# Optimization experiments

Hardware: AMD Instinct MI355X
Metric: run time of the kernel (lower is better)

The kernel has to match this reference:

```python
import jax, jax.numpy as jnp
import numpy as np

B, T, H, D, O = 2, 2048, 16, 64, 1024  # batch, seq, heads, head_size, output_size
E = H * D


def setup_inputs() -> dict:
    key = jax.random.key(0)
    ks = jax.random.split(key, 8)
    return {
        "query": jax.random.normal(ks[0], (B, T, E), jnp.float32),
        "key": jax.random.normal(ks[1], (B, T, E), jnp.float32),
        "value": jax.random.normal(ks[2], (B, T, E), jnp.float32),
        "Wq": jax.random.normal(ks[3], (E, E), jnp.float32) * (E ** -0.5),
        "Wk": jax.random.normal(ks[4], (E, E), jnp.float32) * (E ** -0.5),
        "Wv": jax.random.normal(ks[5], (E, E), jnp.float32) * (E ** -0.5),
        "proj_kernel": jax.random.normal(ks[6], (H, D, O), jnp.float32) * (D ** -0.5),
        "proj_bias": jax.random.normal(ks[7], (O,), jnp.float32),
    }


def reference(query, key, value, Wq, Wk, Wv, proj_kernel, proj_bias):
    # Linear projections (torch nn.Linear: x @ W.T), then split heads
    q = (query @ Wq.T).reshape(B, T, H, D)
    k = (key @ Wk.T).reshape(B, T, H, D)
    v = (value @ Wv.T).reshape(B, T, H, D)
    q = q * (D ** -0.5)  # scale query by 1/sqrt(head_size)
    # logits: [B, H, N, M]
    logits = jnp.einsum("bnhd,bmhd->bhnm", q, k)
    attn_coef = jax.nn.softmax(logits, axis=-1)
    # attn @ V -> [B, N, H, D]
    mh = jnp.einsum("bhnm,bmhd->bnhd", attn_coef, v)
    # custom output projection with per-head kernel [H, D, O]
    out = jnp.einsum("bnhd,hdo->bno", mh, proj_kernel) + proj_bias
    return out, attn_coef
```

## Files before the change

kernel.cpp:

```cpp
#include <hip/hip_runtime.h>
#include <hip/hip_bf16.h>
#include <math.h>

#define B_ 2
#define T_ 2048
#define H_ 16
#define D_ 64
#define E_ 1024
#define O_ 1024
#define BT_ 4096
#define SCALE_Q 0.18033688011f

typedef __attribute__((ext_vector_type(8))) short bf8;
typedef __attribute__((ext_vector_type(4))) float f4;

static __device__ __forceinline__ unsigned short f2bf(float f) {
  unsigned u = __builtin_bit_cast(unsigned, f);
  u += 0x7FFFu + ((u >> 16) & 1u);
  return (unsigned short)(u >> 16);
}

static __device__ __forceinline__ uint4 cvt8(float4 a, float4 b) {
  union { unsigned short s[8]; uint4 v; } u;
  u.s[0] = f2bf(a.x); u.s[1] = f2bf(a.y); u.s[2] = f2bf(a.z); u.s[3] = f2bf(a.w);
  u.s[4] = f2bf(b.x); u.s[5] = f2bf(b.y); u.s[6] = f2bf(b.z); u.s[7] = f2bf(b.w);
  return u.v;
}

static __device__ __forceinline__ f4 mfma16(bf8 a, bf8 b, f4 c) {
  return __builtin_amdgcn_mfma_f32_16x16x32_bf16(a, b, c, 0, 0, 0);
}

static __device__ __forceinline__ float ex2(float x) {
  float r;
  asm("v_exp_f32 %0, %1" : "=v"(r) : "v"(x));
  return r;
}

static __device__ __forceinline__ unsigned cvtpk_bf(float lo, float hi) {
  unsigned r;
  asm("v_cvt_pk_bf16_f32 %0, %1, %2" : "=v"(r) : "v"(lo), "v"(hi));
  return r;
}

__global__ __launch_bounds__(256) void qkv_gemm(const float* __restrict__ Xq,
                                                const float* __restrict__ Xk,
                                                const float* __restrict__ Xv,
                                                const float* __restrict__ Wq,
                                                const float* __restrict__ Wk,
                                                const float* __restrict__ Wv,
                                                unsigned short* __restrict__ dq,
                                                unsigned short* __restrict__ dk,
                                                unsigned short* __restrict__ dv) {
  __shared__ __align__(16) unsigned short lA[64 * 40];
  __shared__ __align__(16) unsigned short lB[128 * 40];
  const int z = blockIdx.z;
  const float* X = (z == 0) ? Xq : (z == 1) ? Xk : Xv;
  const float* W = (z == 0) ? Wq : (z == 1) ? Wk : Wv;
  unsigned short* dst = (z == 0) ? dq : (z == 1) ? dk : dv;
  const float scale = (z == 0) ? SCALE_Q : 1.0f;

  const int tid = threadIdx.x;
  const int bx = blockIdx.x, by = blockIdx.y;
  const int lane = tid & 63, w = tid >> 6;
  const int l15 = lane & 15, qd = lane >> 4;
  const int wr = (w >> 1) * 32, wc = (w & 1) * 64;

  const int ar = tid >> 2, akc = (tid & 3) << 3;
  const int br = tid >> 1, bkc = (tid & 1) << 4;
  const float* aptr = X + (size_t)(bx * 64 + ar) * E_ + akc;
  const float* bptr = W + (size_t)(by * 128 + br) * E_ + bkc;

  f4 acc[2][4];
#pragma unroll
  for (int i = 0; i < 2; ++i)
#pragma unroll
    for (int j = 0; j < 4; ++j) acc[i][j] = (f4){0.f, 0.f, 0.f, 0.f};

  for (int k0 = 0; k0 < E_; k0 += 32) {
    __syncthreads();
    {
      const float4* p = (const float4*)aptr;
      *(uint4*)&lA[ar * 40 + akc] = cvt8(p[0], p[1]);
    }
    {
      const float4* p = (const float4*)bptr;
      *(uint4*)&lB[br * 40 + bkc] = cvt8(p[0], p[1]);
      *(uint4*)&lB[br * 40 + bkc + 8] = cvt8(p[2], p[3]);
    }
    aptr += 32; bptr += 32;
    __syncthreads();

    bf8 af[2], bfr[4];
#pragma unroll
    for (int rt = 0; rt < 2; ++rt)
      af[rt] = *(const bf8*)&lA[(wr + rt * 16 + l15) * 40 + qd * 8];
#pragma unroll
    for (int ct = 0; ct < 4; ++ct)
      bfr[ct] = *(const bf8*)&lB[(wc + ct * 16 + l15) * 40 + qd * 8];
#pragma unroll
    for (int rt = 0; rt < 2; ++rt)
#pragma unroll
      for (int ct = 0; ct < 4; ++ct)
        acc[rt][ct] = mfma16(af[rt], bfr[ct], acc[rt][ct]);
  }

#pragma unroll
  for (int rt = 0; rt < 2; ++rt)
#pragma unroll
    for (int ct = 0; ct < 4; ++ct)
#pragma unroll
      for (int r = 0; r < 4; ++r) {
        int m = bx * 64 + wr + rt * 16 + qd * 4 + r;
        int n = by * 128 + wc + ct * 16 + l15;
        int b = m >> 11, t = m & 2047;
        int h = n >> 6, d = n & 63;
        dst[((size_t)(b * H_ + h) * T_ + t) * D_ + d] = f2bf(acc[rt][ct][r] * scale);
      }
}

__global__ __launch_bounds__(256) void transpose_v(const unsigned short* __restrict__ vh,
                                                   unsigned short* __restrict__ vt) {
  __shared__ __align__(16) unsigned short lT[64 * 72];
  const int tid = threadIdx.x;
  const int bh = blockIdx.x >> 5;
  const int t0 = (blockIdx.x & 31) * 64;
  const unsigned short* src = vh + (size_t)bh * T_ * D_ + (size_t)t0 * D_;
#pragma unroll
  for (int i = 0; i < 2; ++i) {
    int c = tid + i * 256;
    int row = c >> 3, dc = (c & 7) << 3;
    *(uint4*)&lT[row * 72 + dc] = *(const uint4*)(src + row * D_ + dc);
  }
  __syncthreads();
  unsigned short* dstp = vt + (size_t)bh * D_ * T_;
#pragma unroll
  for (int i = 0; i < 2; ++i) {
    int c = tid + i * 256;
    int d = c >> 3, tc = (c & 7) << 3;
    union { unsigned short s[8]; uint4 v; } u;
#pragma unroll
    for (int j = 0; j < 8; ++j) u.s[j] = lT[(tc + j) * 72 + d];
    *(uint4*)(dstp + (size_t)d * T_ + t0 + tc) = u.v;
  }
}

__global__ __launch_bounds__(256) void transpose_proj(const float* __restrict__ pk,
                                                      unsigned short* __restrict__ pt) {
  __shared__ __align__(16) unsigned short lT[64 * 72];
  const int tid = threadIdx.x;
  const int hd0 = (blockIdx.x >> 4) * 64;
  const int o0 = (blockIdx.x & 15) * 64;
#pragma unroll
  for (int i = 0; i < 2; ++i) {
    int c = tid + i * 256;
    int row = c >> 3, oc = (c & 7) << 3;
    const float4* p = (const float4*)(pk + (size_t)(hd0 + row) * O_ + o0 + oc);
    *(uint4*)&lT[row * 72 + oc] = cvt8(p[0], p[1]);
  }
  __syncthreads();
#pragma unroll
  for (int i = 0; i < 2; ++i) {
    int c = tid + i * 256;
    int orow = c >> 3, hc = (c & 7) << 3;
    union { unsigned short s[8]; uint4 v; } u;
#pragma unroll
    for (int j = 0; j < 8; ++j) u.s[j] = lT[(hc + j) * 72 + orow];
    *(uint4*)(pt + (size_t)(o0 + orow) * E_ + hd0 + hc) = u.v;
  }
}

__global__ __launch_bounds__(256) void attention(const unsigned short* __restrict__ qh,
                                                 const unsigned short* __restrict__ kh,
                                                 const unsigned short* __restrict__ vt,
                                                 float* __restrict__ attn,
                                                 unsigned short* __restrict__ mh) {
  __shared__ __align__(16) unsigned short lK[64 * 72];
  __shared__ __align__(16) unsigned short lV[64 * 72];
  __shared__ __align__(16) unsigned short lP[4 * 16 * 72];

  const int tid = threadIdx.x;
  const int bh = blockIdx.x >> 5;
  const int n0 = (blockIdx.x & 31) * 64;
  const int lane = tid & 63, w = tid >> 6;
  const int l15 = lane & 15, qd = lane >> 4;

  const unsigned short* qbase = qh + ((size_t)bh * T_ + n0) * D_;
  const unsigned short* kbase = kh + (size_t)bh * T_ * D_;
  const unsigned short* vbase = vt + (size_t)bh * D_ * T_;

  const bf8 aq0 = *(const bf8*)(qbase + (w * 16 + l15) * D_ + qd * 8);
  const bf8 aq1 = *(const bf8*)(qbase + (w * 16 + l15) * D_ + 32 + qd * 8);

  const int srow = tid >> 3, scol = (tid & 7) << 3;

  float mL = -INFINITY, lL = 0.f;
  for (int m0 = 0; m0 < T_; m0 += 64) {
    __syncthreads();
#pragma unroll
    for (int i = 0; i < 2; ++i) {
      int row = srow + i * 32;
      *(uint4*)&lK[row * 72 + scol] = *(const uint4*)(kbase + (size_t)(m0 + row) * D_ + scol);
    }
    __syncthreads();
    f4 s[4];
#pragma unroll
    for (int kk = 0; kk < 4; ++kk) {
      bf8 k0 = *(const bf8*)&lK[(kk * 16 + l15) * 72 + qd * 8];
      bf8 k1 = *(const bf8*)&lK[(kk * 16 + l15) * 72 + 32 + qd * 8];
      f4 t = (f4){0.f, 0.f, 0.f, 0.f};
      t = mfma16(k0, aq0, t);
      t = mfma16(k1, aq1, t);
      s[kk] = t;
    }
    float tm = s[0][0];
#pragma unroll
    for (int kk = 0; kk < 4; ++kk)
#pragma unroll
      for (int r = 0; r < 4; ++r) tm = fmaxf(tm, s[kk][r]);
    float nm = fmaxf(mL, tm);
    lL *= ex2(mL - nm);
    mL = nm;
#pragma unroll
    for (int kk = 0; kk < 4; ++kk)
#pragma unroll
      for (int r = 0; r < 4; ++r) lL += ex2(s[kk][r] - mL);
  }

  float mrow = mL, lrow = lL;
#pragma unroll
  for (int off = 16; off < 64; off <<= 1) {
    float om = __shfl_xor(mrow, off);
    float ol = __shfl_xor(lrow, off);
    float nm = fmaxf(mrow, om);
    lrow = lrow * ex2(mrow - nm) + ol * ex2(om - nm);
    mrow = nm;
  }
  const float invl = 1.0f / lrow;

  f4 o[4];
#pragma unroll
  for (int dt = 0; dt < 4; ++dt) o[dt] = (f4){0.f, 0.f, 0.f, 0.f};

  float* attnrow = attn + ((size_t)bh * T_ + n0 + w * 16 + l15) * T_ + qd * 4;
  unsigned short* lPw = lP + w * 16 * 72;

  for (int m0 = 0; m0 < T_; m0 += 64) {
    __syncthreads();
#pragma unroll
    for (int i = 0; i < 2; ++i) {
      int row = srow + i * 32;
      *(uint4*)&lK[row * 72 + scol] = *(const uint4*)(kbase + (size_t)(m0 + row) * D_ + scol);
      *(uint4*)&lV[row * 72 + scol] = *(const uint4*)(vbase + (size_t)row * T_ + m0 + scol);
    }
    __syncthreads();
    f4 s[4];
#pragma unroll
    for (int kk = 0; kk < 4; ++kk) {
      bf8 k0 = *(const bf8*)&lK[(kk * 16 + l15) * 72 + qd * 8];
      bf8 k1 = *(const bf8*)&lK[(kk * 16 + l15) * 72 + 32 + qd * 8];
      f4 t = (f4){0.f, 0.f, 0.f, 0.f};
      t = mfma16(k0, aq0, t);
      t = mfma16(k1, aq1, t);
      s[kk] = t;
    }
#pragma unroll
    for (int kk = 0; kk < 4; ++kk) {
      float p0 = ex2(s[kk][0] - mrow) * invl;
      float p1 = ex2(s[kk][1] - mrow) * invl;
      float p2 = ex2(s[kk][2] - mrow) * invl;
      float p3 = ex2(s[kk][3] - mrow) * invl;
      f4 pf = (f4){p0, p1, p2, p3};
      __builtin_nontemporal_store(pf, (f4*)(attnrow + m0 + kk * 16));
      uint2 pb;
      pb.x = cvtpk_bf(p0, p1);
      pb.y = cvtpk_bf(p2, p3);
      *(uint2*)&lPw[l15 * 72 + kk * 16 + qd * 4] = pb;
    }
    bf8 ap0 = *(const bf8*)&lPw[l15 * 72 + qd * 8];
    bf8 ap1 = *(const bf8*)&lPw[l15 * 72 + 32 + qd * 8];
#pragma unroll
    for (int dt = 0; dt < 4; ++dt) {
      bf8 bv0 = *(const bf8*)&lV[(dt * 16 + l15) * 72 + qd * 8];
      bf8 bv1 = *(const bf8*)&lV[(dt * 16 + l15) * 72 + 32 + qd * 8];
      o[dt] = mfma16(ap0, bv0, o[dt]);
      o[dt] = mfma16(ap1, bv1, o[dt]);
    }
  }

  const int b = bh >> 4, h = bh & 15;
#pragma unroll
  for (int dt = 0; dt < 4; ++dt)
#pragma unroll
    for (int r = 0; r < 4; ++r) {
      int t = n0 + w * 16 + qd * 4 + r;
      int d = dt * 16 + l15;
      mh[(size_t)(b * T_ + t) * E_ + h * D_ + d] = f2bf(o[dt][r]);
    }
}

__global__ __launch_bounds__(256) void out_gemm(const unsigned short* __restrict__ A,
                                                const unsigned short* __restrict__ Bm,
                                                const float* __restrict__ bias,
                                                float* __restrict__ Cout) {
  __shared__ __align__(16) unsigned short lA[64 * 40];
  __shared__ __align__(16) unsigned short lB[128 * 40];
  const int tid = threadIdx.x;
  const int bx = blockIdx.x, by = blockIdx.y;
  const int lane = tid & 63, w = tid >> 6;
  const int l15 = lane & 15, qd = lane >> 4;
  const int wr = (w >> 1) * 32, wc = (w & 1) * 64;

  const int ar = tid >> 2, akc = (tid & 3) << 3;
  const unsigned short* aptr = A + (size_t)(bx * 64 + ar) * E_ + akc;

  f4 acc[2][4];
#pragma unroll
  for (int i = 0; i < 2; ++i)
#pragma unroll
    for (int j = 0; j < 4; ++j) acc[i][j] = (f4){0.f, 0.f, 0.f, 0.f};

  for (int k0 = 0; k0 < E_; k0 += 32) {
    __syncthreads();
    *(uint4*)&lA[ar * 40 + akc] = *(const uint4*)aptr;
#pragma unroll
    for (int i = 0; i < 2; ++i) {
      int c = tid + i * 256;
      int br = c >> 2, bkc = (c & 3) << 3;
      *(uint4*)&lB[br * 40 + bkc] =
          *(const uint4*)(Bm + (size_t)(by * 128 + br) * E_ + k0 + bkc);
    }
    aptr += 32;
    __syncthreads();

    bf8 af[2], bfr[4];
#pragma unroll
    for (int rt = 0; rt < 2; ++rt)
      af[rt] = *(const bf8*)&lA[(wr + rt * 16 + l15) * 40 + qd * 8];
#pragma unroll
    for (int ct = 0; ct < 4; ++ct)
      bfr[ct] = *(const bf8*)&lB[(wc + ct * 16 + l15) * 40 + qd * 8];
#pragma unroll
    for (int rt = 0; rt < 2; ++rt)
#pragma unroll
      for (int ct = 0; ct < 4; ++ct)
        acc[rt][ct] = mfma16(af[rt], bfr[ct], acc[rt][ct]);
  }

#pragma unroll
  for (int ct = 0; ct < 4; ++ct) {
    int n = by * 128 + wc + ct * 16 + l15;
    float bv = bias[n];
#pragma unroll
    for (int rt = 0; rt < 2; ++rt)
#pragma unroll
      for (int r = 0; r < 4; ++r) {
        int m = bx * 64 + wr + rt * 16 + qd * 4 + r;
        __builtin_nontemporal_store(acc[rt][ct][r] + bv, &Cout[(size_t)m * O_ + n]);
      }
  }
}

extern "C" void kernel_launch(void* const* d_in, const int* in_sizes, int n_in,
                              void* d_out, int out_size, void* d_ws, size_t ws_size,
                              hipStream_t stream) {
  const float* query = (const float*)d_in[0];
  const float* key_i = (const float*)d_in[1];
  const float* value = (const float*)d_in[2];
  const float* Wq = (const float*)d_in[3];
  const float* Wk = (const float*)d_in[4];
  const float* Wv = (const float*)d_in[5];
  const float* pk = (const float*)d_in[6];
  const float* pb = (const float*)d_in[7];

  float* out = (float*)d_out;
  float* attn = out + (size_t)BT_ * O_;

  unsigned short* ws = (unsigned short*)d_ws;
  unsigned short* qh = ws;
  unsigned short* kh = qh + (size_t)4194304;
  unsigned short* vh = kh + (size_t)4194304;
  unsigned short* vtb = vh + (size_t)4194304;
  unsigned short* pt = vtb + (size_t)4194304;
  unsigned short* mhb = vh;

  dim3 blk(256, 1, 1);
  hipLaunchKernelGGL(qkv_gemm, dim3(64, 8, 3), blk, 0, stream,
                     query, key_i, value, Wq, Wk, Wv, qh, kh, vh);
  hipLaunchKernelGGL(transpose_v, dim3(1024), blk, 0, stream, vh, vtb);
  hipLaunchKernelGGL(transpose_proj, dim3(256), blk, 0, stream, pk, pt);
  hipLaunchKernelGGL(attention, dim3(1024), blk, 0, stream, qh, kh, vtb, attn, mhb);
  hipLaunchKernelGGL(out_gemm, dim3(64, 8), blk, 0, stream, mhb, pt, pb, out);
}
```

Measured before the change: 794.9 us.

## Double attention query tile to 128 rows with 512-thread blocks, merge transposes

The attention kernel now runs 8 waves per block, each covering 128 query rows. Every K/V tile staged in LDS is therefore reused by twice as many queries, and each thread loads one row instead of two. The two transpose kernels are merged into one launch with a branch on block index, and the fp32-to-bf16 conversion uses packed cvt instructions. The cost is fewer blocks (512) and more LDS and register pressure per block, which may reduce occupancy.

```diff
diff --git a/kernel.cpp b/kernel.cpp
--- a/kernel.cpp
+++ b/kernel.cpp
@@ -20,11 +20,19 @@
   return (unsigned short)(u >> 16);
 }
 
+static __device__ __forceinline__ unsigned cvtpk_bf(float lo, float hi) {
+  unsigned r;
+  asm("v_cvt_pk_bf16_f32 %0, %1, %2" : "=v"(r) : "v"(lo), "v"(hi));
+  return r;
+}
+
 static __device__ __forceinline__ uint4 cvt8(float4 a, float4 b) {
-  union { unsigned short s[8]; uint4 v; } u;
-  u.s[0] = f2bf(a.x); u.s[1] = f2bf(a.y); u.s[2] = f2bf(a.z); u.s[3] = f2bf(a.w);
-  u.s[4] = f2bf(b.x); u.s[5] = f2bf(b.y); u.s[6] = f2bf(b.z); u.s[7] = f2bf(b.w);
-  return u.v;
+  uint4 v;
+  v.x = cvtpk_bf(a.x, a.y);
+  v.y = cvtpk_bf(a.z, a.w);
+  v.z = cvtpk_bf(b.x, b.y);
+  v.w = cvtpk_bf(b.z, b.w);
+  return v;
 }
 
 static __device__ __forceinline__ f4 mfma16(bf8 a, bf8 b, f4 c) {
@@ -34,12 +42,6 @@
 static __device__ __forceinline__ float ex2(float x) {
   float r;
   asm("v_exp_f32 %0, %1" : "=v"(r) : "v"(x));
-  return r;
-}
-
-static __device__ __forceinline__ unsigned cvtpk_bf(float lo, float hi) {
-  unsigned r;
-  asm("v_cvt_pk_bf16_f32 %0, %1, %2" : "=v"(r) : "v"(lo), "v"(hi));
   return r;
 }
 
@@ -119,69 +121,69 @@
       }
 }
 
-__global__ __launch_bounds__(256) void transpose_v(const unsigned short* __restrict__ vh,
-                                                   unsigned short* __restrict__ vt) {
+__global__ __launch_bounds__(256) void transpose_all(const unsigned short* __restrict__ vh,
+                                                     unsigned short* __restrict__ vt,
+                                                     const float* __restrict__ pk,
+                                                     unsigned short* __restrict__ pt) {
   __shared__ __align__(16) unsigned short lT[64 * 72];
   const int tid = threadIdx.x;
-  const int bh = blockIdx.x >> 5;
-  const int t0 = (blockIdx.x & 31) * 64;
-  const unsigned short* src = vh + (size_t)bh * T_ * D_ + (size_t)t0 * D_;
-#pragma unroll
-  for (int i = 0; i < 2; ++i) {
-    int c = tid + i * 256;
-    int row = c >> 3, dc = (c & 7) << 3;
-    *(uint4*)&lT[row * 72 + dc] = *(const uint4*)(src + row * D_ + dc);
-  }
-  __syncthreads();
-  unsigned short* dstp = vt + (size_t)bh * D_ * T_;
-#pragma unroll
-  for (int i = 0; i < 2; ++i) {
-    int c = tid + i * 256;
-    int d = c >> 3, tc = (c & 7) << 3;
-    union { unsigned short s[8]; uint4 v; } u;
-#pragma unroll
-    for (int j = 0; j < 8; ++j) u.s[j] = lT[(tc + j) * 72 + d];
-    *(uint4*)(dstp + (size_t)d * T_ + t0 + tc) = u.v;
-  }
-}
-
-__global__ __launch_bounds__(256) void transpose_proj(const float* __restrict__ pk,
-                                                      unsigned short* __restrict__ pt) {
-  __shared__ __align__(16) unsigned short lT[64 * 72];
-  const int tid = threadIdx.x;
-  const int hd0 = (blockIdx.x >> 4) * 64;
-  const int o0 = (blockIdx.x & 15) * 64;
-#pragma unroll
-  for (int i = 0; i < 2; ++i) {
-    int c = tid + i * 256;
-    int row = c >> 3, oc = (c & 7) << 3;
-    const float4* p = (const float4*)(pk + (size_t)(hd0 + row) * O_ + o0 + oc);
-    *(uint4*)&lT[row * 72 + oc] = cvt8(p[0], p[1]);
-  }
-  __syncthreads();
-#pragma unroll
-  for (int i = 0; i < 2; ++i) {
-    int c = tid + i * 256;
-    int orow = c >> 3, hc = (c & 7) << 3;
-    union { unsigned short s[8]; uint4 v; } u;
-#pragma unroll
-    for (int j = 0; j < 8; ++j) u.s[j] = lT[(hc + j) * 72 + orow];
-    *(uint4*)(pt + (size_t)(o0 + orow) * E_ + hd0 + hc) = u.v;
-  }
-}
-
-__global__ __launch_bounds__(256) void attention(const unsigned short* __restrict__ qh,
+  if (blockIdx.x < 1024) {
+    const int bh = blockIdx.x >> 5;
+    const int t0 = (blockIdx.x & 31) * 64;
+    const unsigned short* src = vh + (size_t)bh * T_ * D_ + (size_t)t0 * D_;
+#pragma unroll
+    for (int i = 0; i < 2; ++i) {
+      int c = tid + i * 256;
+      int row = c >> 3, dc = (c & 7) << 3;
+      *(uint4*)&lT[row * 72 + dc] = *(const uint4*)(src + row * D_ + dc);
+    }
+    __syncthreads();
+    unsigned short* dstp = vt + (size_t)bh * D_ * T_;
+#pragma unroll
+    for (int i = 0; i < 2; ++i) {
+      int c = tid + i * 256;
+      int d = c >> 3, tc = (c & 7) << 3;
+      union { unsigned short s[8]; uint4 v; } u;
+#pragma unroll
+      for (int j = 0; j < 8; ++j) u.s[j] = lT[(tc + j) * 72 + d];
+      *(uint4*)(dstp + (size_t)d * T_ + t0 + tc) = u.v;
+    }
+  } else {
+    const int bx = blockIdx.x - 1024;
+    const int hd0 = (bx >> 4) * 64;
+    const int o0 = (bx & 15) * 64;
+#pragma unroll
+    for (int i = 0; i < 2; ++i) {
+      int c = tid + i * 256;
+      int row = c >> 3, oc = (c & 7) << 3;
+      const float4* p = (const float4*)(pk + (size_t)(hd0 + row) * O_ + o0 + oc);
+      *(uint4*)&lT[row * 72 + oc] = cvt8(p[0], p[1]);
+    }
+    __syncthreads();
+#pragma unroll
+    for (int i = 0; i < 2; ++i) {
+      int c = tid + i * 256;
+      int orow = c >> 3, hc = (c & 7) << 3;
+      union { unsigned short s[8]; uint4 v; } u;
+#pragma unroll
+      for (int j = 0; j < 8; ++j) u.s[j] = lT[(hc + j) * 72 + orow];
+      *(uint4*)(pt + (size_t)(o0 + orow) * E_ + hd0 + hc) = u.v;
+    }
+  }
+}
+
+__global__ __launch_bounds__(512) void attention(const unsigned short* __restrict__ qh,
                                                  const unsigned short* __restrict__ kh,
                                                  const unsigned short* __restrict__ vt,
                                                  float* __restrict__ attn,
                                                  unsigned short* __restrict__ mh) {
   __shared__ __align__(16) unsigned short lK[64 * 72];
   __shared__ __align__(16) unsigned short lV[64 * 72];
-  __shared__ __align__(16) unsigned short lP[4 * 16 * 72];
+  __shared__ __align__(16) unsigned short lP[8 * 16 * 72];
 
   const int tid = threadIdx.x;
-  const int bh = blockIdx.x >> 5;
-  const int n0 = (blockIdx.x & 31) * 64;
+  const int bh = blockIdx.x >> 4;
+  const int n0 = (blockIdx.x & 15) * 128;
   const int lane = tid & 63, w = tid >> 6;
   const int l15 = lane & 15, qd = lane >> 4;
 
@@ -197,11 +199,7 @@
   float mL = -INFINITY, lL = 0.f;
   for (int m0 = 0; m0 < T_; m0 += 64) {
     __syncthreads();
-#pragma unroll
-    for (int i = 0; i < 2; ++i) {
-      int row = srow + i * 32;
-      *(uint4*)&lK[row * 72 + scol] = *(const uint4*)(kbase + (size_t)(m0 + row) * D_ + scol);
-    }
+    *(uint4*)&lK[srow * 72 + scol] = *(const uint4*)(kbase + (size_t)(m0 + srow) * D_ + scol);
     __syncthreads();
     f4 s[4];
 #pragma unroll
@@ -247,12 +245,8 @@
 
   for (int m0 = 0; m0 < T_; m0 += 64) {
     __syncthreads();
-#pragma unroll
-    for (int i = 0; i < 2; ++i) {
-      int row = srow + i * 32;
-      *(uint4*)&lK[row * 72 + scol] = *(const uint4*)(kbase + (size_t)(m0 + row) * D_ + scol);
-      *(uint4*)&lV[row * 72 + scol] = *(const uint4*)(vbase + (size_t)row * T_ + m0 + scol);
-    }
+    *(uint4*)&lK[srow * 72 + scol] = *(const uint4*)(kbase + (size_t)(m0 + srow) * D_ + scol);
+    *(uint4*)&lV[srow * 72 + scol] = *(const uint4*)(vbase + (size_t)srow * T_ + m0 + scol);
     __syncthreads();
     f4 s[4];
 #pragma unroll
@@ -387,8 +381,7 @@
   dim3 blk(256, 1, 1);
   hipLaunchKernelGGL(qkv_gemm, dim3(64, 8, 3), blk, 0, stream,
                      query, key_i, value, Wq, Wk, Wv, qh, kh, vh);
-  hipLaunchKernelGGL(transpose_v, dim3(1024), blk, 0, stream, vh, vtb);
-  hipLaunchKernelGGL(transpose_proj, dim3(256), blk, 0, stream, pk, pt);
-  hipLaunchKernelGGL(attention, dim3(1024), blk, 0, stream, qh, kh, vtb, attn, mhb);
+  hipLaunchKernelGGL(transpose_all, dim3(1280), blk, 0, stream, vh, vtb, pk, pt);
+  hipLaunchKernelGGL(attention, dim3(512), dim3(512, 1, 1), 0, stream, qh, kh, vtb, attn, mhb);
   hipLaunchKernelGGL(out_gemm, dim3(64, 8), blk, 0, stream, mhb, pt, pb, out);
 }
```

Measured after the change: 817.8 us. 2.9% more time.
